# Kernel tuning notes

Measured on AMD Instinct MI355X. Metric: run time of the kernel, lower is better.

The kernel has to match this reference:

```python
import jax, jax.numpy as jnp
import numpy as np

N = 50000
E = 800000
IN_C = 256
HID = 256
OUT_C = 128


def _glorot(key, fan_in, fan_out):
    lim = float(np.sqrt(6.0 / (fan_in + fan_out)))
    return jax.random.uniform(key, (fan_in, fan_out), jnp.float32, -lim, lim)


def setup_inputs() -> dict:
    key = jax.random.key(0)
    ks = jax.random.split(key, 10)
    x = jax.random.normal(ks[0], (N, IN_C), dtype=jnp.float32)
    edge_index = jax.random.randint(ks[1], (2, E), 0, N, dtype=jnp.int64)
    return {
        "x": x,
        "edge_index": edge_index,
        # layer 0 MLP: Linear(IN_C,HID)+ReLU+Linear(HID,HID)+ReLU
        "eps0": jnp.zeros((), jnp.float32),
        "W1_0": _glorot(ks[2], IN_C, HID),
        "b1_0": jnp.zeros((HID,), jnp.float32),
        "W2_0": _glorot(ks[3], HID, HID),
        "b2_0": jnp.zeros((HID,), jnp.float32),
        # layer 1 MLP: Linear(HID,HID)+ReLU+Linear(HID,OUT_C)
        "eps1": jnp.zeros((), jnp.float32),
        "W1_1": _glorot(ks[4], HID, HID),
        "b1_1": jnp.zeros((HID,), jnp.float32),
        "W2_1": _glorot(ks[5], HID, OUT_C),
        "b2_1": jnp.zeros((OUT_C,), jnp.float32),
    }


def _gin_layer(x, src, dst, eps, W1, b1, W2, b2, final_relu):
    # sum-aggregate messages x[src] into dst nodes
    agg = jax.ops.segment_sum(x[src], dst, num_segments=N)  # [N, d]
    h = (1.0 + eps) * x + agg
    h = jax.nn.relu(h @ W1 + b1)
    h = h @ W2 + b2
    return jax.nn.relu(h) if final_relu else h


def reference(x, edge_index, eps0, W1_0, b1_0, W2_0, b2_0, eps1, W1_1, b1_1, W2_1, b2_1):
    src, dst = edge_index[0], edge_index[1]
    h = _gin_layer(x, src, dst, eps0, W1_0, b1_0, W2_0, b2_0, final_relu=True)
    h = jax.nn.relu(h)  # model-level ReLU between layers
    h = _gin_layer(h, src, dst, eps1, W1_1, b1_1, W2_1, b2_1, final_relu=False)
    return jax.nn.log_softmax(h, axis=1)
```

## Files before the change

### kernel.cpp

```cpp
#include <hip/hip_runtime.h>

#define FDIM 256
#define OUTC 128
#define CAP  96
#define CURS 16
#define LDA 264
#define MROWS 128

#define QSCALE0 (127.0f / 6.0f)
#define DQ0     (6.0f / 127.0f)

typedef float floatx4 __attribute__((ext_vector_type(4)));
typedef __bf16 bf16x8 __attribute__((ext_vector_type(8)));

__device__ __forceinline__ unsigned short f2bf(float f) {
    union { float f; unsigned u; } v; v.f = f;
    unsigned r = v.u + 0x7FFF + ((v.u >> 16) & 1);
    return (unsigned short)(r >> 16);
}
__device__ __forceinline__ unsigned pack2(float a, float b) {
    return ((unsigned)f2bf(a)) | (((unsigned)f2bf(b)) << 16);
}
__device__ __forceinline__ void add4(float* a, uint2 v) {
    union { unsigned u; float f; } lo, hi;
    lo.u = v.x << 16; hi.u = v.x & 0xffff0000u; a[0] += lo.f; a[1] += hi.f;
    lo.u = v.y << 16; hi.u = v.y & 0xffff0000u; a[2] += lo.f; a[3] += hi.f;
}
__device__ __forceinline__ void addi4(int* a, unsigned u) {
    a[0] += (int)(signed char)(u & 0xffu);
    a[1] += (int)(signed char)((u >> 8) & 0xffu);
    a[2] += (int)(signed char)((u >> 16) & 0xffu);
    a[3] += ((int)u) >> 24;
}
__device__ __forceinline__ int q8(float v) {
    int q = __float2int_rn(v * QSCALE0);
    q = q < -127 ? -127 : (q > 127 ? 127 : q);
    return q & 0xff;
}

__global__ __launch_bounds__(256)
void prep_kernel(const int* __restrict__ src, const int* __restrict__ dst,
                 int* __restrict__ cursor, int* __restrict__ esrc2, int E,
                 const float* __restrict__ x, unsigned char* __restrict__ xq, int total8,
                 const float* __restrict__ W1_0, const float* __restrict__ W2_0,
                 const float* __restrict__ W1_1, const float* __restrict__ W2_1,
                 unsigned short* __restrict__ w1f_0, unsigned short* __restrict__ w2f_0,
                 unsigned short* __restrict__ w1f_1, unsigned short* __restrict__ w2f_1) {
    int gid = blockIdx.x * 256 + threadIdx.x;
    if (gid < E) {
        int d = dst[gid];
        int pos = atomicAdd(&cursor[d * CURS], 1);
        if (pos < CAP) esrc2[d * CAP + pos] = src[gid];
        return;
    }
    gid -= E;
    if (gid < total8) {
        const float4* p = (const float4*)(x + (size_t)gid * 8);
        float4 a = p[0], b = p[1];
        unsigned lo = (unsigned)q8(a.x) | ((unsigned)q8(a.y) << 8) |
                      ((unsigned)q8(a.z) << 16) | ((unsigned)q8(a.w) << 24);
        unsigned hi = (unsigned)q8(b.x) | ((unsigned)q8(b.y) << 8) |
                      ((unsigned)q8(b.z) << 16) | ((unsigned)q8(b.w) << 24);
        *(uint2*)(xq + (size_t)gid * 8) = make_uint2(lo, hi);
        return;
    }
    gid -= total8;
    const int S = FDIM * FDIM;
    const float* W; unsigned short* WF; int local, J, Ncols;
    if (gid < S)          { W = W1_0; WF = w1f_0; local = gid;         J = 4; Ncols = FDIM; }
    else if (gid < 2 * S) { W = W2_0; WF = w2f_0; local = gid - S;     J = 4; Ncols = FDIM; }
    else if (gid < 3 * S) { W = W1_1; WF = w1f_1; local = gid - 2 * S; J = 4; Ncols = FDIM; }
    else if (gid < 3 * S + FDIM * OUTC)
                          { W = W2_1; WF = w2f_1; local = gid - 3 * S; J = 2; Ncols = OUTC; }
    else return;
    int e    = local & 7;
    int lane = (local >> 3) & 63;
    int l15  = lane & 15;
    int quad = lane >> 4;
    int rest = local >> 9;
    int j  = rest % J;  rest /= J;
    int kc = rest & 7;
    int g  = rest >> 3;
    int n = g * (16 * J) + j * 16 + l15;
    int k = kc * 32 + quad * 8 + e;
    WF[local] = f2bf(W[(size_t)k * Ncols + n]);
}

__global__ __launch_bounds__(256)
void gather0_kernel(const unsigned char* __restrict__ xq,
                    const float* __restrict__ xf,
                    const int* __restrict__ esrc2,
                    const int* __restrict__ cursor,
                    const float* __restrict__ epsp, unsigned short* __restrict__ out,
                    int N) {
    int node = __builtin_amdgcn_readfirstlane(
        (int)((blockIdx.x * blockDim.x + threadIdx.x) >> 6));
    int lane = threadIdx.x & 63;
    if (node >= N) return;
    int col = lane * 4;
    int beg = node * CAP;
    int cnt = cursor[node * CURS];
    if (cnt > CAP) cnt = CAP;

    int ai[4] = {0, 0, 0, 0};

    int e = 0;
    for (; e + 16 <= cnt; e += 16) {
        int s[16];
        #pragma unroll
        for (int k = 0; k < 16; ++k) s[k] = esrc2[beg + e + k];
        unsigned v[16];
        #pragma unroll
        for (int k = 0; k < 16; ++k)
            v[k] = *(const unsigned*)(xq + (size_t)s[k] * FDIM + col);
        #pragma unroll
        for (int k = 0; k < 16; ++k) addi4(ai, v[k]);
    }
    int rem = cnt - e;
    if (rem > 0) {
        int s[16];
        #pragma unroll
        for (int k = 0; k < 16; ++k) s[k] = esrc2[beg + e + ((k < rem) ? k : 0)];
        unsigned v[16];
        #pragma unroll
        for (int k = 0; k < 16; ++k)
            v[k] = *(const unsigned*)(xq + (size_t)s[k] * FDIM + col);
        #pragma unroll
        for (int k = 0; k < 16; ++k)
            if (k < rem) addi4(ai, v[k]);
    }

    float scale = 1.0f + *epsp;
    float4 sv = *(const float4*)(xf + (size_t)node * FDIM + col);
    float a4[4];
    a4[0] = (float)ai[0] * DQ0 + scale * sv.x;
    a4[1] = (float)ai[1] * DQ0 + scale * sv.y;
    a4[2] = (float)ai[2] * DQ0 + scale * sv.z;
    a4[3] = (float)ai[3] * DQ0 + scale * sv.w;

    uint2 o;
    o.x = pack2(a4[0], a4[1]);
    o.y = pack2(a4[2], a4[3]);
    *(uint2*)(out + (size_t)node * FDIM + col) = o;
}

__global__ __launch_bounds__(256)
void gather1_kernel(const unsigned short* __restrict__ hb,
                    const int* __restrict__ esrc2,
                    const int* __restrict__ cursor,
                    const float* __restrict__ epsp, unsigned short* __restrict__ out,
                    int N) {
    int node = __builtin_amdgcn_readfirstlane(
        (int)((blockIdx.x * blockDim.x + threadIdx.x) >> 6));
    int lane = threadIdx.x & 63;
    if (node >= N) return;
    int col = lane * 4;
    int beg = node * CAP;
    int cnt = cursor[node * CURS];
    if (cnt > CAP) cnt = CAP;

    float a4[4] = {0.f, 0.f, 0.f, 0.f};

    int e = 0;
    for (; e + 16 <= cnt; e += 16) {
        int s[16];
        #pragma unroll
        for (int k = 0; k < 16; ++k) s[k] = esrc2[beg + e + k];
        uint2 v[16];
        #pragma unroll
        for (int k = 0; k < 16; ++k)
            v[k] = *(const uint2*)(hb + (size_t)s[k] * FDIM + col);
        #pragma unroll
        for (int k = 0; k < 16; ++k) add4(a4, v[k]);
    }
    int rem = cnt - e;
    if (rem > 0) {
        int s[16];
        #pragma unroll
        for (int k = 0; k < 16; ++k) s[k] = esrc2[beg + e + ((k < rem) ? k : 0)];
        uint2 v[16];
        #pragma unroll
        for (int k = 0; k < 16; ++k)
            v[k] = *(const uint2*)(hb + (size_t)s[k] * FDIM + col);
        #pragma unroll
        for (int k = 0; k < 16; ++k)
            if (k < rem) add4(a4, v[k]);
    }

    float scale = 1.0f + *epsp;
    uint2 sv = *(const uint2*)(hb + (size_t)node * FDIM + col);
    union { unsigned u; float f; } t;
    t.u = sv.x << 16;         a4[0] += scale * t.f;
    t.u = sv.x & 0xffff0000u; a4[1] += scale * t.f;
    t.u = sv.y << 16;         a4[2] += scale * t.f;
    t.u = sv.y & 0xffff0000u; a4[3] += scale * t.f;

    uint2 o;
    o.x = pack2(a4[0], a4[1]);
    o.y = pack2(a4[2], a4[3]);
    *(uint2*)(out + (size_t)node * FDIM + col) = o;
}

template<bool FINAL>
__global__ __launch_bounds__(256, 2)
void mlp_fused_kernel(const unsigned short* __restrict__ A,
                      const unsigned short* __restrict__ W1F,
                      const float* __restrict__ b1,
                      const unsigned short* __restrict__ W2F,
                      const float* __restrict__ b2,
                      void* __restrict__ Out, int M) {
    extern __shared__ unsigned short As[];
    float* sred = (float*)(As + MROWS * LDA);

    int tid  = threadIdx.x;
    int wave = tid >> 6;
    int lane = tid & 63;
    int l15  = lane & 15;
    int quad = lane >> 4;
    int row0 = blockIdx.x * MROWS;

    #pragma unroll
    for (int i = 0; i < 16; ++i) {
        int idx = i * 256 + tid;
        int r = idx >> 5;
        int c = (idx & 31) * 8;
        uint4 v = make_uint4(0u, 0u, 0u, 0u);
        int gr = row0 + r;
        if (gr < M) v = *(const uint4*)(A + (size_t)gr * FDIM + c);
        *(uint4*)(As + r * LDA + c) = v;
    }
    __syncthreads();

    floatx4 zero = {0.f, 0.f, 0.f, 0.f};

    {
        floatx4 acc[8][4];
        #pragma unroll
        for (int i = 0; i < 8; ++i)
            #pragma unroll
            for (int j = 0; j < 4; ++j) acc[i][j] = zero;

        const unsigned short* Wb = W1F + (size_t)wave * 16384;
        bf16x8 bcur[4], bnxt[4];
        #pragma unroll
        for (int j = 0; j < 4; ++j)
            bcur[j] = *(const bf16x8*)(Wb + j * 512 + lane * 8);

        for (int kc = 0; kc < 8; ++kc) {
            const unsigned short* Wn = Wb + ((kc < 7) ? (kc + 1) : kc) * 2048;
            #pragma unroll
            for (int j = 0; j < 4; ++j)
                bnxt[j] = *(const bf16x8*)(Wn + j * 512 + lane * 8);
            int k = kc * 32;
            #pragma unroll
            for (int i = 0; i < 8; ++i) {
                bf16x8 af = *(const bf16x8*)(As + (i * 16 + l15) * LDA + k + quad * 8);
                #pragma unroll
                for (int j = 0; j < 4; ++j)
                    acc[i][j] = __builtin_amdgcn_mfma_f32_16x16x32_bf16(
                        af, bcur[j], acc[i][j], 0, 0, 0);
            }
            #pragma unroll
            for (int j = 0; j < 4; ++j) bcur[j] = bnxt[j];
        }

        __syncthreads();

        #pragma unroll
        for (int j = 0; j < 4; ++j) {
            int col = wave * 64 + j * 16 + l15;
            float bv = b1[col];
            #pragma unroll
            for (int i = 0; i < 8; ++i) {
                #pragma unroll
                for (int r = 0; r < 4; ++r) {
                    float v = fmaxf(acc[i][j][r] + bv, 0.f);
                    As[(i * 16 + quad * 4 + r) * LDA + col] = f2bf(v);
                }
            }
        }
    }
    __syncthreads();

    if (!FINAL) {
        floatx4 acc[8][4];
        #pragma unroll
        for (int i = 0; i < 8; ++i)
            #pragma unroll
            for (int j = 0; j < 4; ++j) acc[i][j] = zero;

        const unsigned short* Wb = W2F + (size_t)wave * 16384;
        bf16x8 bcur[4], bnxt[4];
        #pragma unroll
        for (int j = 0; j < 4; ++j)
            bcur[j] = *(const bf16x8*)(Wb + j * 512 + lane * 8);

        for (int kc = 0; kc < 8; ++kc) {
            const unsigned short* Wn = Wb + ((kc < 7) ? (kc + 1) : kc) * 2048;
            #pragma unroll
            for (int j = 0; j < 4; ++j)
                bnxt[j] = *(const bf16x8*)(Wn + j * 512 + lane * 8);
            int k = kc * 32;
            #pragma unroll
            for (int i = 0; i < 8; ++i) {
                bf16x8 af = *(const bf16x8*)(As + (i * 16 + l15) * LDA + k + quad * 8);
                #pragma unroll
                for (int j = 0; j < 4; ++j)
                    acc[i][j] = __builtin_amdgcn_mfma_f32_16x16x32_bf16(
                        af, bcur[j], acc[i][j], 0, 0, 0);
            }
            #pragma unroll
            for (int j = 0; j < 4; ++j) bcur[j] = bnxt[j];
        }

        unsigned short* O = (unsigned short*)Out;
        #pragma unroll
        for (int j = 0; j < 4; ++j) {
            int col = wave * 64 + j * 16 + l15;
            float bv = b2[col];
            #pragma unroll
            for (int i = 0; i < 8; ++i) {
                #pragma unroll
                for (int r = 0; r < 4; ++r) {
                    int grow = row0 + i * 16 + quad * 4 + r;
                    if (grow < M) {
                        float v = fmaxf(acc[i][j][r] + bv, 0.f);
                        O[(size_t)grow * FDIM + col] = f2bf(v);
                    }
                }
            }
        }
    } else {
        floatx4 acc[8][2];
        #pragma unroll
        for (int i = 0; i < 8; ++i)
            #pragma unroll
            for (int j = 0; j < 2; ++j) acc[i][j] = zero;

        const unsigned short* Wb = W2F + (size_t)wave * 8192;
        bf16x8 bcur[2], bnxt[2];
        #pragma unroll
        for (int j = 0; j < 2; ++j)
            bcur[j] = *(const bf16x8*)(Wb + j * 512 + lane * 8);

        for (int kc = 0; kc < 8; ++kc) {
            const unsigned short* Wn = Wb + ((kc < 7) ? (kc + 1) : kc) * 1024;
            #pragma unroll
            for (int j = 0; j < 2; ++j)
                bnxt[j] = *(const bf16x8*)(Wn + j * 512 + lane * 8);
            int k = kc * 32;
            #pragma unroll
            for (int i = 0; i < 8; ++i) {
                bf16x8 af = *(const bf16x8*)(As + (i * 16 + l15) * LDA + k + quad * 8);
                #pragma unroll
                for (int j = 0; j < 2; ++j)
                    acc[i][j] = __builtin_amdgcn_mfma_f32_16x16x32_bf16(
                        af, bcur[j], acc[i][j], 0, 0, 0);
            }
            #pragma unroll
            for (int j = 0; j < 2; ++j) bcur[j] = bnxt[j];
        }

        #pragma unroll
        for (int j = 0; j < 2; ++j) {
            float bv = b2[wave * 32 + j * 16 + l15];
            #pragma unroll
            for (int i = 0; i < 8; ++i)
                #pragma unroll
                for (int r = 0; r < 4; ++r) acc[i][j][r] += bv;
        }

        float* smax = sred;
        float* ssum = sred + MROWS * 4;

        #pragma unroll
        for (int i = 0; i < 8; ++i) {
            #pragma unroll
            for (int r = 0; r < 4; ++r) {
                float m = fmaxf(acc[i][0][r], acc[i][1][r]);
                #pragma unroll
                for (int off = 1; off < 16; off <<= 1) m = fmaxf(m, __shfl_xor(m, off));
                int row = i * 16 + quad * 4 + r;
                if (l15 == 0) smax[row * 4 + wave] = m;
            }
        }
        __syncthreads();

        float Mloc[8][4];
        #pragma unroll
        for (int i = 0; i < 8; ++i) {
            #pragma unroll
            for (int r = 0; r < 4; ++r) {
                int row = i * 16 + quad * 4 + r;
                float Mr = fmaxf(fmaxf(smax[row * 4 + 0], smax[row * 4 + 1]),
                                 fmaxf(smax[row * 4 + 2], smax[row * 4 + 3]));
                Mloc[i][r] = Mr;
                float s = __expf(acc[i][0][r] - Mr) + __expf(acc[i][1][r] - Mr);
                #pragma unroll
                for (int off = 1; off < 16; off <<= 1) s += __shfl_xor(s, off);
                if (l15 == 0) ssum[row * 4 + wave] = s;
            }
        }
        __syncthreads();

        float* O = (float*)Out;
        #pragma unroll
        for (int i = 0; i < 8; ++i) {
            #pragma unroll
            for (int r = 0; r < 4; ++r) {
                int row = i * 16 + quad * 4 + r;
                int grow = row0 + row;
                if (grow < M) {
                    float lse = Mloc[i][r] +
                        __logf(ssum[row * 4 + 0] + ssum[row * 4 + 1] +
                               ssum[row * 4 + 2] + ssum[row * 4 + 3]);
                    #pragma unroll
                    for (int j = 0; j < 2; ++j) {
                        int col = wave * 32 + j * 16 + l15;
                        O[(size_t)grow * OUTC + col] = acc[i][j][r] - lse;
                    }
                }
            }
        }
    }
}

extern "C" void kernel_launch(void* const* d_in, const int* in_sizes, int n_in,
                              void* d_out, int out_size, void* d_ws, size_t ws_size,
                              hipStream_t stream) {
    const float* x    = (const float*)d_in[0];
    const int*   ei   = (const int*)d_in[1];
    const float* eps0 = (const float*)d_in[2];
    const float* W1_0 = (const float*)d_in[3];
    const float* b1_0 = (const float*)d_in[4];
    const float* W2_0 = (const float*)d_in[5];
    const float* b2_0 = (const float*)d_in[6];
    const float* eps1 = (const float*)d_in[7];
    const float* W1_1 = (const float*)d_in[8];
    const float* b1_1 = (const float*)d_in[9];
    const float* W2_1 = (const float*)d_in[10];
    const float* b2_1 = (const float*)d_in[11];
    float* out = (float*)d_out;

    const int N = in_sizes[0] / FDIM;
    const int E = in_sizes[1] / 2;
    const int* src = ei;
    const int* dst = ei + E;

    size_t buf_elems = (size_t)N * FDIM;
    unsigned short* agg = (unsigned short*)d_ws;
    unsigned short* h2  = agg + buf_elems;
    unsigned short* w1f_0 = h2 + buf_elems;
    unsigned short* w2f_0 = w1f_0 + FDIM * FDIM;
    unsigned short* w1f_1 = w2f_0 + FDIM * FDIM;
    unsigned short* w2f_1 = w1f_1 + FDIM * FDIM;
    unsigned char* xq = (unsigned char*)(w2f_1 + FDIM * OUTC);
    int* cursor = (int*)(xq + buf_elems);
    int* esrc2  = cursor + (size_t)N * CURS;

    int gather_blocks = (N + 3) / 4;
    int mlp_blocks = (N + MROWS - 1) / MROWS;
    int total8 = (int)(buf_elems / 8);
    int wtot = 3 * FDIM * FDIM + FDIM * OUTC;
    int prep_threads = E + total8 + wtot;
    size_t mlp_lds = (size_t)MROWS * LDA * 2 + (size_t)MROWS * 4 * 2 * 4;

    hipMemsetAsync(cursor, 0, (size_t)N * CURS * sizeof(int), stream);
    prep_kernel<<<(prep_threads + 255) / 256, 256, 0, stream>>>(
        src, dst, cursor, esrc2, E, x, xq, total8,
        W1_0, W2_0, W1_1, W2_1, w1f_0, w2f_0, w1f_1, w2f_1);

    gather0_kernel<<<gather_blocks, 256, 0, stream>>>(
        xq, x, esrc2, cursor, eps0, agg, N);
    mlp_fused_kernel<false><<<mlp_blocks, 256, mlp_lds, stream>>>(
        agg, w1f_0, b1_0, w2f_0, b2_0, h2, N);

    gather1_kernel<<<gather_blocks, 256, 0, stream>>>(
        h2, esrc2, cursor, eps1, agg, N);
    mlp_fused_kernel<true><<<mlp_blocks, 256, mlp_lds, stream>>>(
        agg, w1f_1, b1_1, w2f_1, b2_1, out, N);
}
```

Baseline: 322.3 us.

## Quantize hidden activations to per-row int8 and compress edge indices to 16-bit

Layer-0 MLP output is now written as int8 with a per-row scale instead of bf16, so the second gather reads a quarter of the bytes per neighbor. Both gathers share one kernel that scales each neighbor row. The self term also comes from the quantized row rather than full-precision x. Edge source indices are stored as uint16 and loaded 16 at a time with vector loads. This cuts gather memory traffic, at the cost of more quantization error. Indices above 65535 would also break, but N=50000 fits.

```diff
diff --git a/kernel.cpp b/kernel.cpp
--- a/kernel.cpp
+++ b/kernel.cpp
@@ -7,9 +7,6 @@
 #define LDA 264
 #define MROWS 128
 
-#define QSCALE0 (127.0f / 6.0f)
-#define DQ0     (6.0f / 127.0f)
-
 typedef float floatx4 __attribute__((ext_vector_type(4)));
 typedef __bf16 bf16x8 __attribute__((ext_vector_type(8)));
 
@@ -21,27 +18,17 @@
 __device__ __forceinline__ unsigned pack2(float a, float b) {
     return ((unsigned)f2bf(a)) | (((unsigned)f2bf(b)) << 16);
 }
-__device__ __forceinline__ void add4(float* a, uint2 v) {
-    union { unsigned u; float f; } lo, hi;
-    lo.u = v.x << 16; hi.u = v.x & 0xffff0000u; a[0] += lo.f; a[1] += hi.f;
-    lo.u = v.y << 16; hi.u = v.y & 0xffff0000u; a[2] += lo.f; a[3] += hi.f;
-}
-__device__ __forceinline__ void addi4(int* a, unsigned u) {
-    a[0] += (int)(signed char)(u & 0xffu);
-    a[1] += (int)(signed char)((u >> 8) & 0xffu);
-    a[2] += (int)(signed char)((u >> 16) & 0xffu);
-    a[3] += ((int)u) >> 24;
-}
-__device__ __forceinline__ int q8(float v) {
-    int q = __float2int_rn(v * QSCALE0);
+__device__ __forceinline__ int q8r(float v, float rs) {
+    int q = __float2int_rn(v * rs);
     q = q < -127 ? -127 : (q > 127 ? 127 : q);
     return q & 0xff;
 }
 
 __global__ __launch_bounds__(256)
 void prep_kernel(const int* __restrict__ src, const int* __restrict__ dst,
-                 int* __restrict__ cursor, int* __restrict__ esrc2, int E,
-                 const float* __restrict__ x, unsigned char* __restrict__ xq, int total8,
+                 int* __restrict__ cursor, unsigned short* __restrict__ esrc2, int E,
+                 const float* __restrict__ x, unsigned char* __restrict__ xq,
+                 float* __restrict__ xs0, int total8,
                  const float* __restrict__ W1_0, const float* __restrict__ W2_0,
                  const float* __restrict__ W1_1, const float* __restrict__ W2_1,
                  unsigned short* __restrict__ w1f_0, unsigned short* __restrict__ w2f_0,
@@ -50,18 +37,24 @@
     if (gid < E) {
         int d = dst[gid];
         int pos = atomicAdd(&cursor[d * CURS], 1);
-        if (pos < CAP) esrc2[d * CAP + pos] = src[gid];
+        if (pos < CAP) esrc2[d * CAP + pos] = (unsigned short)src[gid];
         return;
     }
     gid -= E;
     if (gid < total8) {
         const float4* p = (const float4*)(x + (size_t)gid * 8);
         float4 a = p[0], b = p[1];
-        unsigned lo = (unsigned)q8(a.x) | ((unsigned)q8(a.y) << 8) |
-                      ((unsigned)q8(a.z) << 16) | ((unsigned)q8(a.w) << 24);
-        unsigned hi = (unsigned)q8(b.x) | ((unsigned)q8(b.y) << 8) |
-                      ((unsigned)q8(b.z) << 16) | ((unsigned)q8(b.w) << 24);
+        float m = fmaxf(fmaxf(fmaxf(fabsf(a.x), fabsf(a.y)), fmaxf(fabsf(a.z), fabsf(a.w))),
+                        fmaxf(fmaxf(fabsf(b.x), fabsf(b.y)), fmaxf(fabsf(b.z), fabsf(b.w))));
+        #pragma unroll
+        for (int off = 1; off < 32; off <<= 1) m = fmaxf(m, __shfl_xor(m, off));
+        float rs = (m > 0.f) ? 127.0f / m : 0.f;
+        unsigned lo = (unsigned)q8r(a.x, rs) | ((unsigned)q8r(a.y, rs) << 8) |
+                      ((unsigned)q8r(a.z, rs) << 16) | ((unsigned)q8r(a.w, rs) << 24);
+        unsigned hi = (unsigned)q8r(b.x, rs) | ((unsigned)q8r(b.y, rs) << 8) |
+                      ((unsigned)q8r(b.z, rs) << 16) | ((unsigned)q8r(b.w, rs) << 24);
         *(uint2*)(xq + (size_t)gid * 8) = make_uint2(lo, hi);
+        if ((threadIdx.x & 31) == 0) xs0[gid >> 5] = m * (1.0f / 127.0f);
         return;
     }
     gid -= total8;
@@ -87,12 +80,12 @@
 }
 
 __global__ __launch_bounds__(256)
-void gather0_kernel(const unsigned char* __restrict__ xq,
-                    const float* __restrict__ xf,
-                    const int* __restrict__ esrc2,
-                    const int* __restrict__ cursor,
-                    const float* __restrict__ epsp, unsigned short* __restrict__ out,
-                    int N) {
+void gather_q8_kernel(const unsigned char* __restrict__ q,
+                      const float* __restrict__ qs,
+                      const unsigned short* __restrict__ esrc2,
+                      const int* __restrict__ cursor,
+                      const float* __restrict__ epsp,
+                      unsigned short* __restrict__ out, int N) {
     int node = __builtin_amdgcn_readfirstlane(
         (int)((blockIdx.x * blockDim.x + threadIdx.x) >> 6));
     int lane = threadIdx.x & 63;
@@ -102,98 +95,67 @@
     int cnt = cursor[node * CURS];
     if (cnt > CAP) cnt = CAP;
 
-    int ai[4] = {0, 0, 0, 0};
+    float a4[4] = {0.f, 0.f, 0.f, 0.f};
 
     int e = 0;
     for (; e + 16 <= cnt; e += 16) {
-        int s[16];
-        #pragma unroll
-        for (int k = 0; k < 16; ++k) s[k] = esrc2[beg + e + k];
+        const uint4* ip = (const uint4*)(esrc2 + beg + e);
+        uint4 i0 = ip[0], i1 = ip[1];
+        unsigned iw[8] = {i0.x, i0.y, i0.z, i0.w, i1.x, i1.y, i1.z, i1.w};
+        int s[16]; float sc[16];
+        #pragma unroll
+        for (int m = 0; m < 8; ++m) {
+            s[2*m]   = __builtin_amdgcn_readfirstlane((int)(iw[m] & 0xffffu));
+            s[2*m+1] = __builtin_amdgcn_readfirstlane((int)(iw[m] >> 16));
+        }
+        #pragma unroll
+        for (int k = 0; k < 16; ++k) sc[k] = qs[s[k]];
         unsigned v[16];
         #pragma unroll
         for (int k = 0; k < 16; ++k)
-            v[k] = *(const unsigned*)(xq + (size_t)s[k] * FDIM + col);
-        #pragma unroll
-        for (int k = 0; k < 16; ++k) addi4(ai, v[k]);
+            v[k] = *(const unsigned*)(q + (size_t)s[k] * FDIM + col);
+        #pragma unroll
+        for (int k = 0; k < 16; ++k) {
+            a4[0] = fmaf(sc[k], (float)(int)(signed char)(v[k] & 0xffu), a4[0]);
+            a4[1] = fmaf(sc[k], (float)(int)(signed char)((v[k] >> 8) & 0xffu), a4[1]);
+            a4[2] = fmaf(sc[k], (float)(int)(signed char)((v[k] >> 16) & 0xffu), a4[2]);
+            a4[3] = fmaf(sc[k], (float)((int)v[k] >> 24), a4[3]);
+        }
     }
     int rem = cnt - e;
     if (rem > 0) {
-        int s[16];
-        #pragma unroll
-        for (int k = 0; k < 16; ++k) s[k] = esrc2[beg + e + ((k < rem) ? k : 0)];
+        const uint4* ip = (const uint4*)(esrc2 + beg + e);
+        uint4 i0 = ip[0], i1 = ip[1];
+        unsigned iw[8] = {i0.x, i0.y, i0.z, i0.w, i1.x, i1.y, i1.z, i1.w};
+        int s[16]; float sc[16];
+        #pragma unroll
+        for (int m = 0; m < 8; ++m) {
+            s[2*m]   = __builtin_amdgcn_readfirstlane((int)(iw[m] & 0xffffu));
+            s[2*m+1] = __builtin_amdgcn_readfirstlane((int)(iw[m] >> 16));
+        }
+        #pragma unroll
+        for (int k = 0; k < 16; ++k) if (k >= rem) s[k] = s[0];
+        #pragma unroll
+        for (int k = 0; k < 16; ++k) sc[k] = qs[s[k]];
         unsigned v[16];
         #pragma unroll
         for (int k = 0; k < 16; ++k)
-            v[k] = *(const unsigned*)(xq + (size_t)s[k] * FDIM + col);
-        #pragma unroll
-        for (int k = 0; k < 16; ++k)
-            if (k < rem) addi4(ai, v[k]);
-    }
-
-    float scale = 1.0f + *epsp;
-    float4 sv = *(const float4*)(xf + (size_t)node * FDIM + col);
-    float a4[4];
-    a4[0] = (float)ai[0] * DQ0 + scale * sv.x;
-    a4[1] = (float)ai[1] * DQ0 + scale * sv.y;
-    a4[2] = (float)ai[2] * DQ0 + scale * sv.z;
-    a4[3] = (float)ai[3] * DQ0 + scale * sv.w;
-
-    uint2 o;
-    o.x = pack2(a4[0], a4[1]);
-    o.y = pack2(a4[2], a4[3]);
-    *(uint2*)(out + (size_t)node * FDIM + col) = o;
-}
-
-__global__ __launch_bounds__(256)
-void gather1_kernel(const unsigned short* __restrict__ hb,
-                    const int* __restrict__ esrc2,
-                    const int* __restrict__ cursor,
-                    const float* __restrict__ epsp, unsigned short* __restrict__ out,
-                    int N) {
-    int node = __builtin_amdgcn_readfirstlane(
-        (int)((blockIdx.x * blockDim.x + threadIdx.x) >> 6));
-    int lane = threadIdx.x & 63;
-    if (node >= N) return;
-    int col = lane * 4;
-    int beg = node * CAP;
-    int cnt = cursor[node * CURS];
-    if (cnt > CAP) cnt = CAP;
-
-    float a4[4] = {0.f, 0.f, 0.f, 0.f};
-
-    int e = 0;
-    for (; e + 16 <= cnt; e += 16) {
-        int s[16];
-        #pragma unroll
-        for (int k = 0; k < 16; ++k) s[k] = esrc2[beg + e + k];
-        uint2 v[16];
-        #pragma unroll
-        for (int k = 0; k < 16; ++k)
-            v[k] = *(const uint2*)(hb + (size_t)s[k] * FDIM + col);
-        #pragma unroll
-        for (int k = 0; k < 16; ++k) add4(a4, v[k]);
-    }
-    int rem = cnt - e;
-    if (rem > 0) {
-        int s[16];
-        #pragma unroll
-        for (int k = 0; k < 16; ++k) s[k] = esrc2[beg + e + ((k < rem) ? k : 0)];
-        uint2 v[16];
-        #pragma unroll
-        for (int k = 0; k < 16; ++k)
-            v[k] = *(const uint2*)(hb + (size_t)s[k] * FDIM + col);
-        #pragma unroll
-        for (int k = 0; k < 16; ++k)
-            if (k < rem) add4(a4, v[k]);
-    }
-
-    float scale = 1.0f + *epsp;
-    uint2 sv = *(const uint2*)(hb + (size_t)node * FDIM + col);
-    union { unsigned u; float f; } t;
-    t.u = sv.x << 16;         a4[0] += scale * t.f;
-    t.u = sv.x & 0xffff0000u; a4[1] += scale * t.f;
-    t.u = sv.y << 16;         a4[2] += scale * t.f;
-    t.u = sv.y & 0xffff0000u; a4[3] += scale * t.f;
+            v[k] = *(const unsigned*)(q + (size_t)s[k] * FDIM + col);
+        #pragma unroll
+        for (int k = 0; k < 16; ++k) if (k < rem) {
+            a4[0] = fmaf(sc[k], (float)(int)(signed char)(v[k] & 0xffu), a4[0]);
+            a4[1] = fmaf(sc[k], (float)(int)(signed char)((v[k] >> 8) & 0xffu), a4[1]);
+            a4[2] = fmaf(sc[k], (float)(int)(signed char)((v[k] >> 16) & 0xffu), a4[2]);
+            a4[3] = fmaf(sc[k], (float)((int)v[k] >> 24), a4[3]);
+        }
+    }
+
+    float ssc = qs[node] * (1.0f + *epsp);
+    unsigned sv = *(const unsigned*)(q + (size_t)node * FDIM + col);
+    a4[0] = fmaf(ssc, (float)(int)(signed char)(sv & 0xffu), a4[0]);
+    a4[1] = fmaf(ssc, (float)(int)(signed char)((sv >> 8) & 0xffu), a4[1]);
+    a4[2] = fmaf(ssc, (float)(int)(signed char)((sv >> 16) & 0xffu), a4[2]);
+    a4[3] = fmaf(ssc, (float)((int)sv >> 24), a4[3]);
 
     uint2 o;
     o.x = pack2(a4[0], a4[1]);
@@ -208,7 +170,8 @@
                       const float* __restrict__ b1,
                       const unsigned short* __restrict__ W2F,
                       const float* __restrict__ b2,
-                      void* __restrict__ Out, int M) {
+                      void* __restrict__ Out,
+                      float* __restrict__ xsp, int M) {
     extern __shared__ unsigned short As[];
     float* sred = (float*)(As + MROWS * LDA);
 
@@ -313,21 +276,59 @@
             for (int j = 0; j < 4; ++j) bcur[j] = bnxt[j];
         }
 
-        unsigned short* O = (unsigned short*)Out;
         #pragma unroll
         for (int j = 0; j < 4; ++j) {
-            int col = wave * 64 + j * 16 + l15;
-            float bv = b2[col];
-            #pragma unroll
-            for (int i = 0; i < 8; ++i) {
-                #pragma unroll
-                for (int r = 0; r < 4; ++r) {
-                    int grow = row0 + i * 16 + quad * 4 + r;
-                    if (grow < M) {
-                        float v = fmaxf(acc[i][j][r] + bv, 0.f);
-                        O[(size_t)grow * FDIM + col] = f2bf(v);
-                    }
+            float bv = b2[wave * 64 + j * 16 + l15];
+            #pragma unroll
+            for (int i = 0; i < 8; ++i)
+                #pragma unroll
+                for (int r = 0; r < 4; ++r)
+                    acc[i][j][r] = fmaxf(acc[i][j][r] + bv, 0.f);
+        }
+        #pragma unroll
+        for (int i = 0; i < 8; ++i) {
+            #pragma unroll
+            for (int r = 0; r < 4; ++r) {
+                float m = fmaxf(fmaxf(acc[i][0][r], acc[i][1][r]),
+                                fmaxf(acc[i][2][r], acc[i][3][r]));
+                #pragma unroll
+                for (int off = 1; off < 16; off <<= 1) m = fmaxf(m, __shfl_xor(m, off));
+                int row = i * 16 + quad * 4 + r;
+                if (l15 == 0) sred[row * 4 + wave] = m;
+            }
+        }
+        __syncthreads();
+
+        unsigned char* Bq = (unsigned char*)As;
+        #pragma unroll
+        for (int i = 0; i < 8; ++i) {
+            #pragma unroll
+            for (int r = 0; r < 4; ++r) {
+                int row = i * 16 + quad * 4 + r;
+                float Mr = fmaxf(fmaxf(sred[row * 4 + 0], sred[row * 4 + 1]),
+                                 fmaxf(sred[row * 4 + 2], sred[row * 4 + 3]));
+                float rs = (Mr > 0.f) ? 127.0f / Mr : 0.f;
+                if (wave == 0 && l15 == 0 && row0 + row < M)
+                    xsp[row0 + row] = Mr * (1.0f / 127.0f);
+                #pragma unroll
+                for (int j = 0; j < 4; ++j) {
+                    int col = wave * 64 + j * 16 + l15;
+                    Bq[row * FDIM + col] =
+                        (unsigned char)__float2int_rn(acc[i][j][r] * rs);
                 }
+            }
+        }
+        __syncthreads();
+
+        unsigned char* Oq = (unsigned char*)Out;
+        #pragma unroll
+        for (int it = 0; it < 8; ++it) {
+            int u4 = it * 256 + tid;
+            int r = u4 >> 4;
+            int gr = row0 + r;
+            if (gr < M) {
+                uint4 v = *(uint4*)(Bq + u4 * 16);
+                *(uint4*)(Oq + (size_t)gr * FDIM + (u4 & 15) * 16) = v;
             }
         }
     } else {
@@ -448,15 +449,17 @@
     const int* dst = ei + E;
 
     size_t buf_elems = (size_t)N * FDIM;
-    unsigned short* agg = (unsigned short*)d_ws;
-    unsigned short* h2  = agg + buf_elems;
-    unsigned short* w1f_0 = h2 + buf_elems;
+    unsigned short* agg   = (unsigned short*)d_ws;
+    float*          xs0   = (float*)(agg + buf_elems);
+    float*          xs1   = xs0 + N;
+    int*            cursor= (int*)(xs1 + N);
+    unsigned short* esrc2 = (unsigned short*)(cursor + (size_t)N * CURS);
+    unsigned short* w1f_0 = esrc2 + (size_t)N * CAP;
     unsigned short* w2f_0 = w1f_0 + FDIM * FDIM;
     unsigned short* w1f_1 = w2f_0 + FDIM * FDIM;
     unsigned short* w2f_1 = w1f_1 + FDIM * FDIM;
-    unsigned char* xq = (unsigned char*)(w2f_1 + FDIM * OUTC);
-    int* cursor = (int*)(xq + buf_elems);
-    int* esrc2  = cursor + (size_t)N * CURS;
+    unsigned char*  xq    = (unsigned char*)(w2f_1 + FDIM * OUTC);
+    unsigned char*  h2q   = xq + buf_elems;
 
     int gather_blocks = (N + 3) / 4;
     int mlp_blocks = (N + MROWS - 1) / MROWS;
@@ -467,16 +470,16 @@
 
     hipMemsetAsync(cursor, 0, (size_t)N * CURS * sizeof(int), stream);
     prep_kernel<<<(prep_threads + 255) / 256, 256, 0, stream>>>(
-        src, dst, cursor, esrc2, E, x, xq, total8,
+        src, dst, cursor, esrc2, E, x, xq, xs0, total8,
         W1_0, W2_0, W1_1, W2_1, w1f_0, w2f_0, w1f_1, w2f_1);
 
-    gather0_kernel<<<gather_blocks, 256, 0, stream>>>(
-        xq, x, esrc2, cursor, eps0, agg, N);
+    gather_q8_kernel<<<gather_blocks, 256, 0, stream>>>(
+        xq, xs0, esrc2, cursor, eps0, agg, N);
     mlp_fused_kernel<false><<<mlp_blocks, 256, mlp_lds, stream>>>(
-        agg, w1f_0, b1_0, w2f_0, b2_0, h2, N);
-
-    gather1_kernel<<<gather_blocks, 256, 0, stream>>>(
-        h2, esrc2, cursor, eps1, agg, N);
+        agg, w1f_0, b1_0, w2f_0, b2_0, h2q, xs1, N);
+
+    gather_q8_kernel<<<gather_blocks, 256, 0, stream>>>(
+        h2q, xs1, esrc2, cursor, eps1, agg, N);
     mlp_fused_kernel<true><<<mlp_blocks, 256, mlp_lds, stream>>>(
-        agg, w1f_1, b1_1, w2f_1, b2_1, out, N);
-}
+        agg, w1f_1, b1_1, w2f_1, b2_1, out, nullptr, N);
+}
```

New measurement: 306.4 us. 4.9% less time.
